# Optimization experiments

Hardware: AMD Instinct MI355X
Metric: run time of the kernel (lower is better)

The kernel has to match this reference:

```python
import jax, jax.numpy as jnp
import numpy as np

N = 8192
F = 128

def setup_inputs() -> dict:
    key = jax.random.key(0)
    k1, k2, k3 = jax.random.split(key, 3)
    x = jax.random.normal(k1, (N, F), dtype=jnp.float32)
    adj = jax.random.uniform(k2, (N, N), dtype=jnp.float32)
    # xavier-uniform style init for weight [F, F]
    limit = float(np.sqrt(6.0 / (F + F)))
    weight = jax.random.uniform(k3, (F, F), dtype=jnp.float32, minval=-limit, maxval=limit)
    return {"x": x, "adj": adj, "weight": weight}

def reference(x, adj, weight):
    # adj_hat = adj + I
    n = adj.shape[0]
    adj_hat = adj + jnp.eye(n, dtype=adj.dtype)
    # degree vector; D^{-1/2} A_hat D^{-1/2} expressed as row/col scaling
    deg = jnp.sum(adj_hat, axis=1)
    d_inv_sqrt = (deg + 1e-8) ** -0.5  # [N]
    support = d_inv_sqrt[:, None] * adj_hat * d_inv_sqrt[None, :]  # [N, N]
    out = jnp.matmul(jnp.matmul(support, x), weight)  # [N, F]
    return jax.nn.relu(out)
```

## Files before the change

kernel.cpp:

```cpp
#include <hip/hip_runtime.h>
#include <hip/hip_bf16.h>

#define NN 8192
#define FF 128
#define BM 64
#define BK 64
#define KS 8
#define KCH (NN / KS)
#define NSTEP (KCH / BK)

typedef __attribute__((ext_vector_type(8))) short bf16x8;
typedef __attribute__((ext_vector_type(4))) float f32x4;

__device__ __forceinline__ short f2bf(float f) {
  unsigned u = __float_as_uint(f);
  u += 0x7FFFu + ((u >> 16) & 1u);
  return (short)(u >> 16);
}
__device__ __forceinline__ float bf2f(short s) {
  return __uint_as_float(((unsigned)(unsigned short)s) << 16);
}

__global__ __launch_bounds__(256) void k_deg(const float* __restrict__ adj,
                                             float* __restrict__ dinv) {
  const int row = blockIdx.x;
  const float4* p = (const float4*)(adj + (size_t)row * NN);
  float s = 0.f;
#pragma unroll
  for (int it = 0; it < 8; ++it) {
    float4 v = p[it * 256 + threadIdx.x];
    s += (v.x + v.y) + (v.z + v.w);
  }
#pragma unroll
  for (int off = 32; off > 0; off >>= 1) s += __shfl_down(s, off, 64);
  __shared__ float partial[4];
  if ((threadIdx.x & 63) == 0) partial[threadIdx.x >> 6] = s;
  __syncthreads();
  if (threadIdx.x == 0) {
    float deg = (partial[0] + partial[1]) + (partial[2] + partial[3]) + 1.0f;
    dinv[row] = 1.0f / sqrtf(deg + 1e-8f);
  }
}

__global__ __launch_bounds__(256) void k_scale_t(const float* __restrict__ x,
                                                 const float* __restrict__ dinv,
                                                 short* __restrict__ yT) {
  __shared__ float tile[64][129];
  const int r0 = blockIdx.x * 64;
  const int tid = threadIdx.x;
#pragma unroll
  for (int it = 0; it < 8; ++it) {
    int q = it * 256 + tid;
    int r = q >> 5;
    int c = q & 31;
    float4 v = ((const float4*)(x + (size_t)(r0 + r) * FF))[c];
    float d = dinv[r0 + r];
    tile[r][c * 4 + 0] = v.x * d;
    tile[r][c * 4 + 1] = v.y * d;
    tile[r][c * 4 + 2] = v.z * d;
    tile[r][c * 4 + 3] = v.w * d;
  }
  __syncthreads();
  const int f = tid >> 1;
  const int i0 = (tid & 1) * 32;
#pragma unroll
  for (int g = 0; g < 4; ++g) {
    bf16x8 o;
#pragma unroll
    for (int j = 0; j < 8; ++j) o[j] = f2bf(tile[i0 + g * 8 + j][f]);
    *(bf16x8*)(yT + (size_t)f * NN + r0 + i0 + g * 8) = o;
  }
}

__global__ __launch_bounds__(512, 4) void k_gemm(const float* __restrict__ adj,
                                                 const short* __restrict__ yT,
                                                 float* __restrict__ zpart) {
  __shared__ short As[BM][72];
  __shared__ short Bs[128][72];
  const int tid = threadIdx.x;
  const int wave = tid >> 6;
  const int lane = tid & 63;
  const int mb = 127 - (int)(blockIdx.x & 127);
  const int ks = blockIdx.x >> 7;
  const int row0 = mb * BM;
  const size_t kbase = (size_t)ks * KCH;

  const int s_ar = tid >> 3;
  const int s_ac = (tid & 7) * 8;
  const float* pa = adj + (size_t)(row0 + s_ar) * NN + kbase + s_ac;
  const int s_br = tid >> 3;
  const int s_bc = (tid & 7) * 8;
  const short* pb0 = yT + (size_t)s_br * NN + kbase + s_bc;
  const short* pb1 = yT + (size_t)(s_br + 64) * NN + kbase + s_bc;

  const int wm = (wave >> 2) * 32;
  const int wn = (wave & 3) * 32;
  const int fr = lane & 15;
  const int kh = (lane >> 4) * 8;

  f32x4 acc00 = {0.f,0.f,0.f,0.f}, acc01 = acc00, acc10 = acc00, acc11 = acc00;

  float4 aXlo, aXhi, aYlo, aYhi;
  bf16x8 bX0, bX1, bY0, bY1;

#define LOADT(alo, ahi, b0v, b1v, koff) do {                                   \
    alo = *(const float4*)(pa + (koff));                                       \
    ahi = *(const float4*)(pa + (koff) + 4);                                   \
    b0v = *(const bf16x8*)(pb0 + (koff));                                      \
    b1v = *(const bf16x8*)(pb1 + (koff));                                      \
  } while (0)

#define STAGE(alo, ahi, b0v, b1v) do {                                         \
    bf16x8 ap_;                                                                \
    ap_[0] = f2bf(alo.x); ap_[1] = f2bf(alo.y);                                \
    ap_[2] = f2bf(alo.z); ap_[3] = f2bf(alo.w);                                \
    ap_[4] = f2bf(ahi.x); ap_[5] = f2bf(ahi.y);                                \
    ap_[6] = f2bf(ahi.z); ap_[7] = f2bf(ahi.w);                                \
    *(bf16x8*)&As[s_ar][s_ac] = ap_;                                           \
    *(bf16x8*)&Bs[s_br][s_bc] = b0v;                                           \
    *(bf16x8*)&Bs[s_br + 64][s_bc] = b1v;                                      \
  } while (0)

#define COMPUTE() do {                                                         \
    _Pragma("unroll")                                                          \
    for (int kk = 0; kk < 2; ++kk) {                                           \
      bf16x8 a0 = *(const bf16x8*)&As[wm + fr][kk * 32 + kh];                  \
      bf16x8 a1 = *(const bf16x8*)&As[wm + 16 + fr][kk * 32 + kh];             \
      bf16x8 b0 = *(const bf16x8*)&Bs[wn + fr][kk * 32 + kh];                  \
      bf16x8 b1 = *(const bf16x8*)&Bs[wn + 16 + fr][kk * 32 + kh];             \
      acc00 = __builtin_amdgcn_mfma_f32_16x16x32_bf16(a0, b0, acc00, 0, 0, 0); \
      acc01 = __builtin_amdgcn_mfma_f32_16x16x32_bf16(a0, b1, acc01, 0, 0, 0); \
      acc10 = __builtin_amdgcn_mfma_f32_16x16x32_bf16(a1, b0, acc10, 0, 0, 0); \
      acc11 = __builtin_amdgcn_mfma_f32_16x16x32_bf16(a1, b1, acc11, 0, 0, 0); \
    }                                                                          \
  } while (0)

  LOADT(aXlo, aXhi, bX0, bX1, 0);
  LOADT(aYlo, aYhi, bY0, bY1, BK);

  for (int step = 0; step < NSTEP; step += 2) {
    STAGE(aXlo, aXhi, bX0, bX1);
    __syncthreads();
    if (step + 2 < NSTEP) LOADT(aXlo, aXhi, bX0, bX1, (step + 2) * BK);
    COMPUTE();
    __syncthreads();

    STAGE(aYlo, aYhi, bY0, bY1);
    __syncthreads();
    if (step + 3 < NSTEP) LOADT(aYlo, aYhi, bY0, bY1, (step + 3) * BK);
    COMPUTE();
    __syncthreads();
  }

  const int r4 = (lane >> 4) * 4;
  float* zp = zpart + ((size_t)ks << 20);
#pragma unroll
  for (int r = 0; r < 4; ++r) {
    int gi0 = row0 + wm + r4 + r;
    int gi1 = gi0 + 16;
    zp[(size_t)gi0 * FF + wn + fr]      = acc00[r];
    zp[(size_t)gi0 * FF + wn + 16 + fr] = acc01[r];
    zp[(size_t)gi1 * FF + wn + fr]      = acc10[r];
    zp[(size_t)gi1 * FF + wn + 16 + fr] = acc11[r];
  }
#undef LOADT
#undef STAGE
#undef COMPUTE
}

__global__ __launch_bounds__(256) void k_out(const float* __restrict__ zpart,
                                             const float* __restrict__ x,
                                             const float* __restrict__ dinv,
                                             const float* __restrict__ w,
                                             float* __restrict__ out) {
  __shared__ float zs[16][128];
  const int r0 = blockIdx.x * 16;
  const int tid = threadIdx.x;
#pragma unroll
  for (int half = 0; half < 2; ++half) {
    int p = half * 256 + tid;
    int r = p >> 5;
    int c4 = p & 31;
    int gi = r0 + r;
    const float* base = zpart + (size_t)gi * FF + c4 * 4;
    float4 s = *(const float4*)base;
#pragma unroll
    for (int sidx = 1; sidx < KS; ++sidx) {
      float4 v = *(const float4*)(base + ((size_t)sidx << 20));
      s.x += v.x; s.y += v.y; s.z += v.z; s.w += v.w;
    }
    float4 xv = *(const float4*)(x + (size_t)gi * FF + c4 * 4);
    float di = dinv[gi];
    float di2 = di * di;
    zs[r][c4 * 4 + 0] = di * s.x + di2 * xv.x;
    zs[r][c4 * 4 + 1] = di * s.y + di2 * xv.y;
    zs[r][c4 * 4 + 2] = di * s.z + di2 * xv.z;
    zs[r][c4 * 4 + 3] = di * s.w + di2 * xv.w;
  }
  __syncthreads();
  const int f = tid & 127;
  const int rg = (tid >> 7) * 8;
  float acc[8] = {0.f, 0.f, 0.f, 0.f, 0.f, 0.f, 0.f, 0.f};
#pragma unroll 4
  for (int k = 0; k < 128; ++k) {
    float wv = w[k * FF + f];
#pragma unroll
    for (int r = 0; r < 8; ++r) acc[r] += zs[rg + r][k] * wv;
  }
#pragma unroll
  for (int r = 0; r < 8; ++r) {
    out[(size_t)(r0 + rg + r) * FF + f] = fmaxf(acc[r], 0.0f);
  }
}

extern "C" void kernel_launch(void* const* d_in, const int* in_sizes, int n_in,
                              void* d_out, int out_size, void* d_ws, size_t ws_size,
                              hipStream_t stream) {
  const float* x   = (const float*)d_in[0];
  const float* adj = (const float*)d_in[1];
  const float* w   = (const float*)d_in[2];
  float* out = (float*)d_out;

  float* dinv  = (float*)d_ws;
  short* yT    = (short*)((char*)d_ws + 64 * 1024);
  float* zpart = (float*)((char*)d_ws + 4 * 1024 * 1024);

  k_deg    <<<NN,      256, 0, stream>>>(adj, dinv);
  k_scale_t<<<NN / 64, 256, 0, stream>>>(x, dinv, yT);
  k_gemm   <<<128 * KS, 512, 0, stream>>>(adj, yT, zpart);
  k_out    <<<NN / 16, 256, 0, stream>>>(zpart, x, dinv, w, out);
}
```

Measured before the change: 122.2 us.

## Convert adj to bf16 in degree pass and store partial sums as bf16

The degree kernel now also writes a bf16 copy of the adjacency matrix, so the GEMM streams half as many bytes for A and no longer converts fp32 to bf16 in its staging step. The split-K partial results are also written and read as bf16, halving that intermediate traffic. The cost is an extra full-size 128MB write plus re-read of the bf16 matrix, so total adjacency traffic stays about the same. Rounding the partial sums to bf16 also adds accuracy error.

```diff
diff --git a/kernel.cpp b/kernel.cpp
--- a/kernel.cpp
+++ b/kernel.cpp
@@ -21,15 +21,20 @@
   return __uint_as_float(((unsigned)(unsigned short)s) << 16);
 }
 
-__global__ __launch_bounds__(256) void k_deg(const float* __restrict__ adj,
-                                             float* __restrict__ dinv) {
+__global__ __launch_bounds__(256) void k_deg_cvt(const float* __restrict__ adj,
+                                                 float* __restrict__ dinv,
+                                                 short* __restrict__ abf) {
   const int row = blockIdx.x;
   const float4* p = (const float4*)(adj + (size_t)row * NN);
+  short4* q = (short4*)(abf + (size_t)row * NN);
   float s = 0.f;
 #pragma unroll
   for (int it = 0; it < 8; ++it) {
     float4 v = p[it * 256 + threadIdx.x];
     s += (v.x + v.y) + (v.z + v.w);
+    short4 o;
+    o.x = f2bf(v.x); o.y = f2bf(v.y); o.z = f2bf(v.z); o.w = f2bf(v.w);
+    q[it * 256 + threadIdx.x] = o;
   }
 #pragma unroll
   for (int off = 32; off > 0; off >>= 1) s += __shfl_down(s, off, 64);
@@ -72,9 +77,9 @@
   }
 }
 
-__global__ __launch_bounds__(512, 4) void k_gemm(const float* __restrict__ adj,
+__global__ __launch_bounds__(512, 4) void k_gemm(const short* __restrict__ abf,
                                                  const short* __restrict__ yT,
-                                                 float* __restrict__ zpart) {
+                                                 short* __restrict__ zpart) {
   __shared__ short As[BM][72];
   __shared__ short Bs[128][72];
   const int tid = threadIdx.x;
@@ -87,11 +92,9 @@
 
   const int s_ar = tid >> 3;
   const int s_ac = (tid & 7) * 8;
-  const float* pa = adj + (size_t)(row0 + s_ar) * NN + kbase + s_ac;
-  const int s_br = tid >> 3;
-  const int s_bc = (tid & 7) * 8;
-  const short* pb0 = yT + (size_t)s_br * NN + kbase + s_bc;
-  const short* pb1 = yT + (size_t)(s_br + 64) * NN + kbase + s_bc;
+  const short* pa  = abf + (size_t)(row0 + s_ar) * NN + kbase + s_ac;
+  const short* pb0 = yT + (size_t)s_ar * NN + kbase + s_ac;
+  const short* pb1 = yT + (size_t)(s_ar + 64) * NN + kbase + s_ac;
 
   const int wm = (wave >> 2) * 32;
   const int wn = (wave & 3) * 32;
@@ -100,25 +103,18 @@
 
   f32x4 acc00 = {0.f,0.f,0.f,0.f}, acc01 = acc00, acc10 = acc00, acc11 = acc00;
 
-  float4 aXlo, aXhi, aYlo, aYhi;
-  bf16x8 bX0, bX1, bY0, bY1;
-
-#define LOADT(alo, ahi, b0v, b1v, koff) do {                                   \
-    alo = *(const float4*)(pa + (koff));                                       \
-    ahi = *(const float4*)(pa + (koff) + 4);                                   \
+  bf16x8 aX, aY, bX0, bX1, bY0, bY1;
+
+#define LOADT(av, b0v, b1v, koff) do {                                         \
+    av  = *(const bf16x8*)(pa  + (koff));                                      \
     b0v = *(const bf16x8*)(pb0 + (koff));                                      \
     b1v = *(const bf16x8*)(pb1 + (koff));                                      \
   } while (0)
 
-#define STAGE(alo, ahi, b0v, b1v) do {                                         \
-    bf16x8 ap_;                                                                \
-    ap_[0] = f2bf(alo.x); ap_[1] = f2bf(alo.y);                                \
-    ap_[2] = f2bf(alo.z); ap_[3] = f2bf(alo.w);                                \
-    ap_[4] = f2bf(ahi.x); ap_[5] = f2bf(ahi.y);                                \
-    ap_[6] = f2bf(ahi.z); ap_[7] = f2bf(ahi.w);                                \
-    *(bf16x8*)&As[s_ar][s_ac] = ap_;                                           \
-    *(bf16x8*)&Bs[s_br][s_bc] = b0v;                                           \
-    *(bf16x8*)&Bs[s_br + 64][s_bc] = b1v;                                      \
+#define STAGE(av, b0v, b1v) do {                                               \
+    *(bf16x8*)&As[s_ar][s_ac] = av;                                            \
+    *(bf16x8*)&Bs[s_ar][s_ac] = b0v;                                           \
+    *(bf16x8*)&Bs[s_ar + 64][s_ac] = b1v;                                      \
   } while (0)
 
 #define COMPUTE() do {                                                         \
@@ -135,40 +131,40 @@
     }                                                                          \
   } while (0)
 
-  LOADT(aXlo, aXhi, bX0, bX1, 0);
-  LOADT(aYlo, aYhi, bY0, bY1, BK);
+  LOADT(aX, bX0, bX1, 0);
+  LOADT(aY, bY0, bY1, BK);
 
   for (int step = 0; step < NSTEP; step += 2) {
-    STAGE(aXlo, aXhi, bX0, bX1);
-    __syncthreads();
-    if (step + 2 < NSTEP) LOADT(aXlo, aXhi, bX0, bX1, (step + 2) * BK);
+    STAGE(aX, bX0, bX1);
+    __syncthreads();
+    if (step + 2 < NSTEP) LOADT(aX, bX0, bX1, (step + 2) * BK);
     COMPUTE();
     __syncthreads();
 
-    STAGE(aYlo, aYhi, bY0, bY1);
-    __syncthreads();
-    if (step + 3 < NSTEP) LOADT(aYlo, aYhi, bY0, bY1, (step + 3) * BK);
+    STAGE(aY, bY0, bY1);
+    __syncthreads();
+    if (step + 3 < NSTEP) LOADT(aY, bY0, bY1, (step + 3) * BK);
     COMPUTE();
     __syncthreads();
   }
 
   const int r4 = (lane >> 4) * 4;
-  float* zp = zpart + ((size_t)ks << 20);
+  short* zp = zpart + ((size_t)ks << 20);
 #pragma unroll
   for (int r = 0; r < 4; ++r) {
     int gi0 = row0 + wm + r4 + r;
     int gi1 = gi0 + 16;
-    zp[(size_t)gi0 * FF + wn + fr]      = acc00[r];
-    zp[(size_t)gi0 * FF + wn + 16 + fr] = acc01[r];
-    zp[(size_t)gi1 * FF + wn + fr]      = acc10[r];
-    zp[(size_t)gi1 * FF + wn + 16 + fr] = acc11[r];
+    zp[(size_t)gi0 * FF + wn + fr]      = f2bf(acc00[r]);
+    zp[(size_t)gi0 * FF + wn + 16 + fr] = f2bf(acc01[r]);
+    zp[(size_t)gi1 * FF + wn + fr]      = f2bf(acc10[r]);
+    zp[(size_t)gi1 * FF + wn + 16 + fr] = f2bf(acc11[r]);
   }
 #undef LOADT
 #undef STAGE
 #undef COMPUTE
 }
 
-__global__ __launch_bounds__(256) void k_out(const float* __restrict__ zpart,
+__global__ __launch_bounds__(256) void k_out(const short* __restrict__ zpart,
                                              const float* __restrict__ x,
                                              const float* __restrict__ dinv,
                                              const float* __restrict__ w,
@@ -182,20 +178,20 @@
     int r = p >> 5;
     int c4 = p & 31;
     int gi = r0 + r;
-    const float* base = zpart + (size_t)gi * FF + c4 * 4;
-    float4 s = *(const float4*)base;
-#pragma unroll
-    for (int sidx = 1; sidx < KS; ++sidx) {
-      float4 v = *(const float4*)(base + ((size_t)sidx << 20));
-      s.x += v.x; s.y += v.y; s.z += v.z; s.w += v.w;
+    const short* base = zpart + (size_t)gi * FF + c4 * 4;
+    float s0 = 0.f, s1 = 0.f, s2 = 0.f, s3 = 0.f;
+#pragma unroll
+    for (int sidx = 0; sidx < KS; ++sidx) {
+      short4 v = *(const short4*)(base + ((size_t)sidx << 20));
+      s0 += bf2f(v.x); s1 += bf2f(v.y); s2 += bf2f(v.z); s3 += bf2f(v.w);
     }
     float4 xv = *(const float4*)(x + (size_t)gi * FF + c4 * 4);
     float di = dinv[gi];
     float di2 = di * di;
-    zs[r][c4 * 4 + 0] = di * s.x + di2 * xv.x;
-    zs[r][c4 * 4 + 1] = di * s.y + di2 * xv.y;
-    zs[r][c4 * 4 + 2] = di * s.z + di2 * xv.z;
-    zs[r][c4 * 4 + 3] = di * s.w + di2 * xv.w;
+    zs[r][c4 * 4 + 0] = di * s0 + di2 * xv.x;
+    zs[r][c4 * 4 + 1] = di * s1 + di2 * xv.y;
+    zs[r][c4 * 4 + 2] = di * s2 + di2 * xv.z;
+    zs[r][c4 * 4 + 3] = di * s3 + di2 * xv.w;
   }
   __syncthreads();
   const int f = tid & 127;
@@ -223,10 +219,11 @@
 
   float* dinv  = (float*)d_ws;
   short* yT    = (short*)((char*)d_ws + 64 * 1024);
-  float* zpart = (float*)((char*)d_ws + 4 * 1024 * 1024);
-
-  k_deg    <<<NN,      256, 0, stream>>>(adj, dinv);
+  short* zpart = (short*)((char*)d_ws + 4 * 1024 * 1024);
+  short* abf   = (short*)((char*)d_ws + 24 * 1024 * 1024);
+
+  k_deg_cvt<<<NN,      256, 0, stream>>>(adj, dinv, abf);
   k_scale_t<<<NN / 64, 256, 0, stream>>>(x, dinv, yT);
-  k_gemm   <<<128 * KS, 512, 0, stream>>>(adj, yT, zpart);
+  k_gemm   <<<128 * KS, 512, 0, stream>>>(abf, yT, zpart);
   k_out    <<<NN / 16, 256, 0, stream>>>(zpart, x, dinv, w, out);
 }
```

After: 136.8 us. 1.12x slower.
